# Kernel tuning notes

Measured on AMD Instinct MI355X. Metric: run time of the kernel, lower is better.

Reference implementation:

```python
import jax, jax.numpy as jnp
import numpy as np

N = 50000; E = 1600000; G = 512; HID = 128; H = 4; C = 32
NEG_SLOPE = 0.2


def _seg_softmax(scores, idx, n):
    # scores: [E, H], idx: [E] target nodes; softmax per target segment
    m = jax.ops.segment_max(scores, idx, num_segments=n)
    m = jnp.where(jnp.isfinite(m), m, 0.0)
    e = jnp.exp(scores - m[idx])
    s = jax.ops.segment_sum(e, idx, num_segments=n)
    return e / (s[idx] + 1e-16)


def setup_inputs() -> dict:
    key = jax.random.key(0)
    ks = jax.random.split(key, 32)
    nrm = lambda k, shape: jax.random.normal(k, shape, jnp.float32) * 0.05
    inp = {
        'x_nodes': jax.random.randint(ks[0], (N, 2), 0, 9, dtype=jnp.int32),
        'edge_index': jax.random.randint(ks[1], (2, E), 0, N, dtype=jnp.int32),
        'batch': jnp.sort(jax.random.randint(ks[2], (N,), 0, G, dtype=jnp.int32)),
        'num_graphs': G,
        'emb': nrm(ks[3], (9, 32)),
        'depth_emb': nrm(ks[4], (20, 32)),
        'proj_W': nrm(ks[5], (64, HID)),
        'proj_b': nrm(ks[6], (HID,)),
        'gat_W': nrm(ks[7], (3, HID, H * C)),
        'gat_att_src': nrm(ks[8], (3, H, C)),
        'gat_att_dst': nrm(ks[9], (3, H, C)),
        'gat_bias': nrm(ks[10], (3, HID)),
        'tr_Wq': nrm(ks[11], (HID, H * C)), 'tr_bq': nrm(ks[12], (H * C,)),
        'tr_Wk': nrm(ks[13], (HID, H * C)), 'tr_bk': nrm(ks[14], (H * C,)),
        'tr_Wv': nrm(ks[15], (HID, H * C)), 'tr_bv': nrm(ks[16], (H * C,)),
        'tr_Wskip': nrm(ks[17], (HID, HID)), 'tr_bskip': nrm(ks[18], (HID,)),
        'ln_g': jnp.ones((HID,), jnp.float32),
        'ln_b': jnp.zeros((HID,), jnp.float32),
    }
    return inp


def _forward(x_nodes, edge_index, batch, num_graphs, emb, depth_emb, proj_W, proj_b,
             gat_W, gat_att_src, gat_att_dst, gat_bias,
             tr_Wq, tr_bq, tr_Wk, tr_bk, tr_Wv, tr_bv, tr_Wskip, tr_bskip, ln_g, ln_b):
    n = x_nodes.shape[0]
    node_e = emb[x_nodes[:, 0]]                      # [N,32]
    depth_e = depth_emb[jnp.clip(x_nodes[:, 1], 0, 19)]  # [N,32]
    h = jnp.concatenate([node_e, depth_e], axis=1) @ proj_W + proj_b  # [N,128]

    # GATConv adds self-loops by default
    loops = jnp.arange(n, dtype=edge_index.dtype)
    src = jnp.concatenate([edge_index[0], loops])
    dst = jnp.concatenate([edge_index[1], loops])

    for l in range(3):
        hw = (h @ gat_W[l]).reshape(n, H, C)         # [N,H,C]
        a_src = (hw * gat_att_src[l]).sum(-1)        # [N,H]
        a_dst = (hw * gat_att_dst[l]).sum(-1)        # [N,H]
        scores = a_src[src] + a_dst[dst]             # [E+N,H]
        scores = jnp.where(scores >= 0, scores, NEG_SLOPE * scores)
        alpha = _seg_softmax(scores, dst, n)         # [E+N,H]
        msg = hw[src] * alpha[:, :, None]            # [E+N,H,C]
        out = jax.ops.segment_sum(msg, dst, num_segments=n).reshape(n, H * C)
        h = h + jax.nn.elu(out + gat_bias[l])

    # TransformerConv (no self-loops), root_weight=True
    tsrc, tdst = edge_index[0], edge_index[1]
    q = (h @ tr_Wq + tr_bq).reshape(n, H, C)
    k = (h @ tr_Wk + tr_bk).reshape(n, H, C)
    v = (h @ tr_Wv + tr_bv).reshape(n, H, C)
    scores = (q[tdst] * k[tsrc]).sum(-1) / jnp.sqrt(jnp.float32(C))  # [E,H]
    alpha = _seg_softmax(scores, tdst, n)
    agg = jax.ops.segment_sum(v[tsrc] * alpha[:, :, None], tdst, num_segments=n)
    h_trans = agg.reshape(n, H * C) + (h @ tr_Wskip + tr_bskip)
    h = h + jax.nn.elu(h_trans)

    # LayerNorm
    mu = h.mean(-1, keepdims=True)
    var = ((h - mu) ** 2).mean(-1, keepdims=True)
    h = (h - mu) * jax.lax.rsqrt(var + 1e-5) * ln_g + ln_b

    # global_mean_pool
    sums = jax.ops.segment_sum(h, batch, num_segments=num_graphs)
    cnt = jax.ops.segment_sum(jnp.ones((n,), h.dtype), batch, num_segments=num_graphs)
    return sums / jnp.maximum(cnt, 1.0)[:, None]


def reference(x_nodes, edge_index, batch, num_graphs, emb, depth_emb, proj_W, proj_b,
              gat_W, gat_att_src, gat_att_dst, gat_bias,
              tr_Wq, tr_bq, tr_Wk, tr_bk, tr_Wv, tr_bv, tr_Wskip, tr_bskip, ln_g, ln_b):
    return _forward(x_nodes, edge_index, batch, num_graphs, emb, depth_emb, proj_W, proj_b,
                    gat_W, gat_att_src, gat_att_dst, gat_bias,
                    tr_Wq, tr_bq, tr_Wk, tr_bk, tr_Wv, tr_bv, tr_Wskip, tr_bskip, ln_g, ln_b)
```

## Files before the change

kernel.cpp:

```cpp
#include <hip/hip_runtime.h>
#include <hip/hip_bf16.h>

typedef unsigned int uint;
typedef unsigned short ushort;
typedef __attribute__((ext_vector_type(8))) short bf16x8;
typedef __attribute__((ext_vector_type(4))) float f32x4;
typedef __attribute__((ext_vector_type(2))) float f32x2;

__device__ __forceinline__ float2 bf2_to_f2(uint u){
  union {unsigned int i; float f;} a,b;
  a.i = (u & 0xffffu) << 16;
  b.i = u & 0xffff0000u;
  return make_float2(a.f, b.f);
}
__device__ __forceinline__ float b2f(ushort u){
  union{uint i; float f;} x; x.i = (uint)u << 16; return x.f;
}
__device__ __forceinline__ ushort bf16bits(float f){
  union{ __hip_bfloat16 h; ushort u;} x; x.h = __float2bfloat16(f); return x.u;
}
__device__ __forceinline__ uint pack_bf2(float x, float y){
  return ((uint)bf16bits(y)<<16) | (uint)bf16bits(x);
}


__global__ void k_init_h(const int* __restrict__ xn, const float* __restrict__ table,
                         ushort* __restrict__ hb, int n){
  int gid = blockIdx.x*blockDim.x + threadIdx.x;
  if (gid >= n*64) return;
  int node = gid >> 6, lp = gid & 63;
  int x0 = xn[2*node];
  int x1 = xn[2*node+1]; x1 = x1<0?0:(x1>19?19:x1);
  const float* tr = table + (size_t)(x0*20+x1)*128 + lp*2;
  reinterpret_cast<uint*>(hb)[(size_t)node*64 + lp] = pack_bf2(tr[0], tr[1]);
}

__global__ void k_rank(const int* __restrict__ ei, int* __restrict__ cnt,
                       int* __restrict__ rank, int E){
  int e = blockIdx.x*blockDim.x + threadIdx.x;
  if (e >= E) return;
  rank[e] = atomicAdd(&cnt[ei[E+e]], 1);
}

__global__ __launch_bounds__(256) void k_scan_block(const int* __restrict__ deg, int* __restrict__ rowstart,
                                                    int* __restrict__ bsum, int n){
  int tid = threadIdx.x;
  int gid = blockIdx.x*256 + tid;
  int lane = tid & 63, wv = tid >> 6;
  int v = (gid < n) ? deg[gid] : 0;
  int x = v;
  #pragma unroll
  for (int off=1; off<64; off<<=1){
    int t = __shfl_up(x, off);
    if (lane >= off) x += t;
  }
  __shared__ int wsum[4], woff[4];
  if (lane==63) wsum[wv] = x;
  __syncthreads();
  if (tid==0){
    int r = 0;
    for (int i=0;i<4;++i){ woff[i]=r; r += wsum[i]; }
    bsum[blockIdx.x] = r;
  }
  __syncthreads();
  if (gid < n) rowstart[gid] = x + woff[wv] - v;
}

__global__ __launch_bounds__(256) void k_scan_sums(int* __restrict__ bsum, int nb){
  int tid = threadIdx.x;
  int lane = tid&63, wv = tid>>6;
  int v = (tid<nb)?bsum[tid]:0;
  int x = v;
  #pragma unroll
  for (int off=1;off<64;off<<=1){ int t=__shfl_up(x,off); if(lane>=off) x+=t; }
  __shared__ int wsum[4], woff[4];
  if (lane==63) wsum[wv]=x;
  __syncthreads();
  if (tid==0){ int r=0; for(int i=0;i<4;++i){woff[i]=r;r+=wsum[i];} }
  __syncthreads();
  if (tid<nb) bsum[tid] = x + woff[wv] - v;
}

__global__ void k_scan_add(int* __restrict__ rowstart, const int* __restrict__ bsum, int n, int total){
  int gid = blockIdx.x*256 + threadIdx.x;
  if (gid < n) rowstart[gid] += bsum[blockIdx.x];
  if (gid == 0) rowstart[n] = total;
}

__global__ void k_place(const int* __restrict__ ei, const int* __restrict__ rowstart,
                        const int* __restrict__ rank, ushort* __restrict__ csr16, int E){
  int e = blockIdx.x*blockDim.x + threadIdx.x;
  if (e >= E) return;
  csr16[rowstart[ei[E+e]] + rank[e]] = (ushort)ei[e];
}

__global__ __launch_bounds__(256) void k_prep_all(
    const float* __restrict__ gatW, const float* __restrict__ attS, const float* __restrict__ attD,
    const float* __restrict__ Wq, const float* __restrict__ Wk,
    const float* __restrict__ Wv, const float* __restrict__ Ws,
    const float* __restrict__ bq, const float* __restrict__ bk,
    const float* __restrict__ bv, const float* __restrict__ bs,
    const float* __restrict__ emb, const float* __restrict__ demb,
    const float* __restrict__ projW, const float* __restrict__ projB,
    ushort* __restrict__ wt_gat, ushort* __restrict__ wt_qkvs,
    float* __restrict__ bias512, float* __restrict__ table){
  int blk = blockIdx.x, t = threadIdx.x;
  if (blk < 192){
    int i = blk*256 + t;
    int l = i >> 14, rem = i & 16383, c = rem >> 7, k = rem & 127;
    wt_gat[(size_t)l*18432 + c*128 + k] = bf16bits(gatW[l*16384 + k*128 + c]);
  } else if (blk < 216){
    int idx = (blk-192)*256 + t;
    int l = idx >> 11, i16 = (idx >> 7) & 15, k = idx & 127;
    float acc = 0.f;
    if (i16 < 8){
      int sd = i16 >> 2, hh = i16 & 3;
      const float* att = (sd ? attD : attS) + l*128 + hh*32;
      #pragma unroll 8
      for (int c=0;c<32;++c) acc += gatW[l*16384 + k*128 + hh*32 + c] * att[c];
    }
    wt_gat[(size_t)l*18432 + (128+i16)*128 + k] = bf16bits(acc);
  } else if (blk < 472){
    int i = (blk-216)*256 + t;
    int c = i >> 7, k = i & 127;
    const float* W; const float* B; int sc; float scale = 1.f;
    if (c < 128){ W = Wq; B = bq; sc = c; scale = 0.011048543456039805f; }
    else if (c < 384){
      int ct = c >> 7, within = c & 127, cf = within >> 4, cl = within & 15;
      int m = cl + 16*((ct-1)*2 + (cf>>2));
      int wn = cf & 3;
      if (wn < 2){ W = Wk; B = bk; sc = 2*m + wn; }
      else       { W = Wv; B = bv; sc = 2*m + wn - 2; }
    } else { W = Ws; B = bs; sc = c - 384; }
    wt_qkvs[c*128 + k] = bf16bits(W[k*128 + sc] * scale);
    if (k == 0) bias512[c] = B[sc] * scale;
  } else {
    int idx = (blk-472)*256 + t;
    int combo = idx >> 7, d = idx & 127;
    int a = combo/20, b = combo - a*20;
    float acc = projB[d];
    #pragma unroll 8
    for (int i=0;i<32;++i) acc += emb[a*32+i]*projW[i*128+d];
    #pragma unroll 8
    for (int i=0;i<32;++i) acc += demb[b*32+i]*projW[(32+i)*128+d];
    table[combo*128+d] = acc;
  }
}

template<int CT, int MODE>
__global__ __launch_bounds__(256) void k_gemm_mfma(const ushort* __restrict__ X,
        const ushort* __restrict__ Wt, const float* __restrict__ bias,
        void* __restrict__ Yq, uint* __restrict__ Ykv, ushort* __restrict__ Ysk,
        float* __restrict__ Asd, int n){
  constexpr int COLS = (MODE==1) ? 144 : 128;
  constexpr int NCF  = COLS/16;
  __shared__ ushort wl[COLS*136];
  const int t = threadIdx.x;
  const int w = t >> 6, lane = t & 63;
  const int cl = lane & 15, khi = lane >> 4;
  const int rbase = blockIdx.x*64;

  int arow = rbase + w*16 + cl; if (arow >= n) arow = n-1;
  const bf16x8* Xr = reinterpret_cast<const bf16x8*>(X + (size_t)arow*128);
  bf16x8 a0 = Xr[0+khi], a1 = Xr[4+khi], a2 = Xr[8+khi], a3 = Xr[12+khi];

  for (int ct=0; ct<CT; ++ct){
    const ushort* wsrc = Wt + (size_t)ct*16384;
    __syncthreads();
    for (int idx = t; idx < COLS*2; idx += 256){
      int col = idx >> 1, k0 = (idx & 1)*64;
      const bf16x8* src = reinterpret_cast<const bf16x8*>(wsrc + (size_t)col*128 + k0);
      bf16x8* dst = reinterpret_cast<bf16x8*>(wl + col*136 + k0);
      #pragma unroll
      for (int i=0;i<8;++i) dst[i] = src[i];
    }
    __syncthreads();

    f32x4 acc[NCF];
    #pragma unroll
    for (int cf=0;cf<NCF;++cf) acc[cf] = f32x4{0.f,0.f,0.f,0.f};

    #pragma unroll
    for (int ks=0; ks<4; ++ks){
      bf16x8 av = (ks==0)?a0:(ks==1)?a1:(ks==2)?a2:a3;
      #pragma unroll
      for (int cf=0; cf<NCF; ++cf){
        bf16x8 bv = *reinterpret_cast<const bf16x8*>(wl + (cf*16+cl)*136 + ks*32 + khi*8);
        acc[cf] = __builtin_amdgcn_mfma_f32_16x16x32_bf16(av, bv, acc[cf], 0, 0, 0);
      }
    }

    #pragma unroll
    for (int j=0;j<4;++j){
      int node = rbase + w*16 + khi*4 + j;
      if (node < n){
        if (MODE==1){
          unsigned char* Y8 = (unsigned char*)Yq;
          float f0 = acc[0][j]*16.f, f1 = acc[1][j]*16.f, f2 = acc[2][j]*16.f, f3 = acc[3][j]*16.f;
          float f4 = acc[4][j]*16.f, f5 = acc[5][j]*16.f, f6 = acc[6][j]*16.f, f7 = acc[7][j]*16.f;
          int d0 = __builtin_amdgcn_cvt_pk_fp8_f32(f0, f1, 0, false);
          d0     = __builtin_amdgcn_cvt_pk_fp8_f32(f2, f3, d0, true);
          int d1 = __builtin_amdgcn_cvt_pk_fp8_f32(f4, f5, 0, false);
          d1     = __builtin_amdgcn_cvt_pk_fp8_f32(f6, f7, d1, true);
          *reinterpret_cast<uint2*>(Y8 + (size_t)node*128 + cl*8) = make_uint2((uint)d0, (uint)d1);
          if (cl < 8) Asd[(size_t)node*8 + cl] = acc[8][j];
        } else {
          if (ct == 0 || ct == 3){
            ushort* Y = (ct == 0) ? (ushort*)Yq : Ysk;
            ushort* yr = Y + (size_t)node*128 + cl;
            #pragma unroll
            for (int cf=0;cf<8;++cf)
              yr[cf*16] = bf16bits(acc[cf][j] + bias[ct*128 + cf*16 + cl]);
          } else {
            #pragma unroll
            for (int g=0; g<2; ++g){
              float f0 = (acc[g*4+0][j] + bias[ct*128 + (g*4+0)*16 + cl])*16.f;
              float f1 = (acc[g*4+1][j] + bias[ct*128 + (g*4+1)*16 + cl])*16.f;
              float f2 = (acc[g*4+2][j] + bias[ct*128 + (g*4+2)*16 + cl])*16.f;
              float f3 = (acc[g*4+3][j] + bias[ct*128 + (g*4+3)*16 + cl])*16.f;
              int d = __builtin_amdgcn_cvt_pk_fp8_f32(f0, f1, 0, false);
              d     = __builtin_amdgcn_cvt_pk_fp8_f32(f2, f3, d, true);
              int m = cl + 16*((ct-1)*2 + g);
              Ykv[(size_t)node*64 + m] = (uint)d;
            }
          }
        }
      }
    }
  }
}

__global__ __launch_bounds__(256) void k_gat_agg(const int* __restrict__ rowstart, const ushort* __restrict__ csr16,
              const unsigned char* __restrict__ hw8, const float* __restrict__ a_sd,
              const float* __restrict__ bias, ushort* __restrict__ hb, int n){
  __shared__ float4 lw[4][64];
  __shared__ ushort lsrc[4][64];
  int wv = threadIdx.x >> 6, l = threadIdx.x & 63;
  int node = blockIdx.x*4 + wv;
  if (node >= n) return;
  int b = l & 31, half = l >> 5;
  int h0 = (b & 1) * 2;
  int cl = b >> 1;
  int start = rowstart[node], end = rowstart[node+1];
  float4 ad4 = *reinterpret_cast<const float4*>(a_sd + (size_t)node*8 + 4);
  const uint* rows32 = reinterpret_cast<const uint*>(hw8);

  float a0=0.f,a1=0.f,a2=0.f,a3=0.f,sA=0.f,sB=0.f;
  if (half == 0){
    float adA = (h0==0) ? ad4.x : ad4.z;
    float adB = (h0==0) ? ad4.y : ad4.w;
    float scA = a_sd[(size_t)node*8 + h0]     + adA; scA = fmaxf(scA, 0.2f*scA);
    float scB = a_sd[(size_t)node*8 + h0 + 1] + adB; scB = fmaxf(scB, 0.2f*scB);
    float wA = __expf(fminf(scA,30.f));
    float wB = __expf(fminf(scB,30.f));
    uint u = rows32[(size_t)node*32 + b];
    f32x2 flo = __builtin_amdgcn_cvt_pk_f32_fp8((int)u, false);
    f32x2 fhi = __builtin_amdgcn_cvt_pk_f32_fp8((int)u, true);
    sA = wA; sB = wB;
    a0 = wA*flo.x; a1 = wA*flo.y; a2 = wB*fhi.x; a3 = wB*fhi.y;
  }

  const float* lwf = reinterpret_cast<const float*>(&lw[wv][0]);
  for (int base = start; base < end; base += 64){
    int len = end - base; if (len > 64) len = 64;
    if (l < len){
      int sv = csr16[base + l];
      lsrc[wv][l] = (ushort)sv;
      float4 a4 = *reinterpret_cast<const float4*>(a_sd + (size_t)sv*8);
      float s0 = a4.x + ad4.x; s0 = fmaxf(s0, 0.2f*s0);
      float s1 = a4.y + ad4.y; s1 = fmaxf(s1, 0.2f*s1);
      float s2 = a4.z + ad4.z; s2 = fmaxf(s2, 0.2f*s2);
      float s3 = a4.w + ad4.w; s3 = fmaxf(s3, 0.2f*s3);
      float4 w4;
      w4.x = __expf(fminf(s0,30.f));
      w4.y = __expf(fminf(s1,30.f));
      w4.z = __expf(fminf(s2,30.f));
      w4.w = __expf(fminf(s3,30.f));
      lw[wv][l] = w4;
    }
    int p = half;
    for (; p+6 < len; p += 8){
      int e0 = lsrc[wv][p], e1 = lsrc[wv][p+2], e2 = lsrc[wv][p+4], e3 = lsrc[wv][p+6];
      float2 w0 = *reinterpret_cast<const float2*>(lwf + p*4 + h0);
      float2 w1 = *reinterpret_cast<const float2*>(lwf + (p+2)*4 + h0);
      float2 w2 = *reinterpret_cast<const float2*>(lwf + (p+4)*4 + h0);
      float2 w3 = *reinterpret_cast<const float2*>(lwf + (p+6)*4 + h0);
      uint u0 = rows32[(size_t)e0*32 + b];
      uint u1 = rows32[(size_t)e1*32 + b];
      uint u2 = rows32[(size_t)e2*32 + b];
      uint u3 = rows32[(size_t)e3*32 + b];
      f32x2 f;
      f = __builtin_amdgcn_cvt_pk_f32_fp8((int)u0, false); a0 += w0.x*f.x; a1 += w0.x*f.y;
      f = __builtin_amdgcn_cvt_pk_f32_fp8((int)u0, true);  a2 += w0.y*f.x; a3 += w0.y*f.y;
      f = __builtin_amdgcn_cvt_pk_f32_fp8((int)u1, false); a0 += w1.x*f.x; a1 += w1.x*f.y;
      f = __builtin_amdgcn_cvt_pk_f32_fp8((int)u1, true);  a2 += w1.y*f.x; a3 += w1.y*f.y;
      f = __builtin_amdgcn_cvt_pk_f32_fp8((int)u2, false); a0 += w2.x*f.x; a1 += w2.x*f.y;
      f = __builtin_amdgcn_cvt_pk_f32_fp8((int)u2, true);  a2 += w2.y*f.x; a3 += w2.y*f.y;
      f = __builtin_amdgcn_cvt_pk_f32_fp8((int)u3, false); a0 += w3.x*f.x; a1 += w3.x*f.y;
      f = __builtin_amdgcn_cvt_pk_f32_fp8((int)u3, true);  a2 += w3.y*f.x; a3 += w3.y*f.y;
      sA += (w0.x+w1.x)+(w2.x+w3.x);
      sB += (w0.y+w1.y)+(w2.y+w3.y);
    }
    for (; p < len; p += 2){
      int e0 = lsrc[wv][p];
      float2 w0 = *reinterpret_cast<const float2*>(lwf + p*4 + h0);
      uint u0 = rows32[(size_t)e0*32 + b];
      f32x2 f;
      f = __builtin_amdgcn_cvt_pk_f32_fp8((int)u0, false); a0 += w0.x*f.x; a1 += w0.x*f.y;
      f = __builtin_amdgcn_cvt_pk_f32_fp8((int)u0, true);  a2 += w0.y*f.x; a3 += w0.y*f.y;
      sA += w0.x; sB += w0.y;
    }
  }
  a0 += __shfl_xor(a0,32); a1 += __shfl_xor(a1,32);
  a2 += __shfl_xor(a2,32); a3 += __shfl_xor(a3,32);
  sA += __shfl_xor(sA,32); sB += __shfl_xor(sB,32);
  float invA = (1.f/16.f)/(sA + 1e-16f);
  float invB = (1.f/16.f)/(sB + 1e-16f);
  float accx = half ? a2 : a0;
  float accy = half ? a3 : a1;
  float inv  = half ? invB : invA;
  int c0 = (h0*2 + half*2)*16 + cl;
  int c1 = c0 + 16;
  float o0 = accx*inv + bias[c0]; o0 = o0 > 0.f ? o0 : (__expf(o0)-1.f);
  float o1 = accy*inv + bias[c1]; o1 = o1 > 0.f ? o1 : (__expf(o1)-1.f);
  float hx = b2f(hb[(size_t)node*128 + c0]) + o0;
  float hy = b2f(hb[(size_t)node*128 + c1]) + o1;
  hb[(size_t)node*128 + c0] = bf16bits(hx);
  hb[(size_t)node*128 + c1] = bf16bits(hy);
}

__global__ __launch_bounds__(256) void k_trans_agg(const int* __restrict__ rowstart, const ushort* __restrict__ csr16,
              const ushort* __restrict__ yq, const uint* __restrict__ ykv,
              const ushort* __restrict__ ysk, const float* __restrict__ lng,
              const float* __restrict__ lnb, ushort* __restrict__ hb, int n){
  int wv = threadIdx.x>>6, lane = threadIdx.x&63;
  int node = blockIdx.x*4 + wv;
  if (node >= n) return;
  int li = lane & 15;
  bool odd1 = li & 1, odd2 = li & 2;
  int lbase = lane & 48;
  const uint* q32 = reinterpret_cast<const uint*>(yq);
  const uint* s32 = reinterpret_cast<const uint*>(ysk);
  uint* h32 = reinterpret_cast<uint*>(hb);
  float2 q2 = bf2_to_f2(q32[(size_t)node*64 + lane]);
  int start = rowstart[node], end = rowstart[node+1];
  float s = 0.f, s_tail = 0.f, ax = 0.f, ay = 0.f;
  int p = start;
  for (; p+7 < end; p += 8){
    int i0 = csr16[p],   i1 = csr16[p+1], i2 = csr16[p+2], i3 = csr16[p+3];
    int i4 = csr16[p+4], i5 = csr16[p+5], i6 = csr16[p+6], i7 = csr16[p+7];
    uint u0 = ykv[(size_t)i0*64 + lane];
    uint u1 = ykv[(size_t)i1*64 + lane];
    uint u2 = ykv[(size_t)i2*64 + lane];
    uint u3 = ykv[(size_t)i3*64 + lane];
    uint u4 = ykv[(size_t)i4*64 + lane];
    uint u5 = ykv[(size_t)i5*64 + lane];
    uint u6 = ykv[(size_t)i6*64 + lane];
    uint u7 = ykv[(size_t)i7*64 + lane];
    f32x2 k0 = __builtin_amdgcn_cvt_pk_f32_fp8((int)u0, false);
    f32x2 k1 = __builtin_amdgcn_cvt_pk_f32_fp8((int)u1, false);
    f32x2 k2 = __builtin_amdgcn_cvt_pk_f32_fp8((int)u2, false);
    f32x2 k3 = __builtin_amdgcn_cvt_pk_f32_fp8((int)u3, false);
    float p0 = q2.x*k0.x + q2.y*k0.y;
    float p1 = q2.x*k1.x + q2.y*k1.y;
    float p2 = q2.x*k2.x + q2.y*k2.y;
    float p3 = q2.x*k3.x + q2.y*k3.y;
    float aA = (odd1 ? p1 : p0) + __shfl_xor(odd1 ? p0 : p1, 1);
    float bA = (odd1 ? p3 : p2) + __shfl_xor(odd1 ? p2 : p3, 1);
    float cA = (odd2 ? bA : aA) + __shfl_xor(odd2 ? aA : bA, 2);
    cA += __shfl_xor(cA, 4);
    cA += __shfl_xor(cA, 8);
    float wA = __expf(fminf(cA, 30.f));
    f32x2 k4 = __builtin_amdgcn_cvt_pk_f32_fp8((int)u4, false);
    f32x2 k5 = __builtin_amdgcn_cvt_pk_f32_fp8((int)u5, false);
    f32x2 k6 = __builtin_amdgcn_cvt_pk_f32_fp8((int)u6, false);
    f32x2 k7 = __builtin_amdgcn_cvt_pk_f32_fp8((int)u7, false);
    float p4 = q2.x*k4.x + q2.y*k4.y;
    float p5 = q2.x*k5.x + q2.y*k5.y;
    float p6 = q2.x*k6.x + q2.y*k6.y;
    float p7 = q2.x*k7.x + q2.y*k7.y;
    float aB = (odd1 ? p5 : p4) + __shfl_xor(odd1 ? p4 : p5, 1);
    float bB = (odd1 ? p7 : p6) + __shfl_xor(odd1 ? p6 : p7, 1);
    float cB = (odd2 ? bB : aB) + __shfl_xor(odd2 ? aB : bB, 2);
    cB += __shfl_xor(cB, 4);
    cB += __shfl_xor(cB, 8);
    float wB = __expf(fminf(cB, 30.f));
    s += wA + wB;
    float w0 = __shfl(wA, lbase);
    float w1 = __shfl(wA, lbase|1);
    float w2 = __shfl(wA, lbase|2);
    float w3 = __shfl(wA, lbase|3);
    float w4 = __shfl(wB, lbase);
    float w5 = __shfl(wB, lbase|1);
    float w6 = __shfl(wB, lbase|2);
    float w7 = __shfl(wB, lbase|3);
    f32x2 v0 = __builtin_amdgcn_cvt_pk_f32_fp8((int)u0, true);
    f32x2 v1 = __builtin_amdgcn_cvt_pk_f32_fp8((int)u1, true);
    f32x2 v2 = __builtin_amdgcn_cvt_pk_f32_fp8((int)u2, true);
    f32x2 v3 = __builtin_amdgcn_cvt_pk_f32_fp8((int)u3, true);
    f32x2 v4 = __builtin_amdgcn_cvt_pk_f32_fp8((int)u4, true);
    f32x2 v5 = __builtin_amdgcn_cvt_pk_f32_fp8((int)u5, true);
    f32x2 v6 = __builtin_amdgcn_cvt_pk_f32_fp8((int)u6, true);
    f32x2 v7 = __builtin_amdgcn_cvt_pk_f32_fp8((int)u7, true);
    ax += w0*v0.x + w1*v1.x + w2*v2.x + w3*v3.x
        + w4*v4.x + w5*v5.x + w6*v6.x + w7*v7.x;
    ay += w0*v0.y + w1*v1.y + w2*v2.y + w3*v3.y
        + w4*v4.y + w5*v5.y + w6*v6.y + w7*v7.y;
  }
  for (; p+3 < end; p += 4){
    int i0 = csr16[p], i1 = csr16[p+1], i2 = csr16[p+2], i3 = csr16[p+3];
    uint u0 = ykv[(size_t)i0*64 + lane];
    uint u1 = ykv[(size_t)i1*64 + lane];
    uint u2 = ykv[(size_t)i2*64 + lane];
    uint u3 = ykv[(size_t)i3*64 + lane];
    f32x2 k0 = __builtin_amdgcn_cvt_pk_f32_fp8((int)u0, false);
    f32x2 k1 = __builtin_amdgcn_cvt_pk_f32_fp8((int)u1, false);
    f32x2 k2 = __builtin_amdgcn_cvt_pk_f32_fp8((int)u2, false);
    f32x2 k3 = __builtin_amdgcn_cvt_pk_f32_fp8((int)u3, false);
    float p0 = q2.x*k0.x + q2.y*k0.y;
    float p1 = q2.x*k1.x + q2.y*k1.y;
    float p2 = q2.x*k2.x + q2.y*k2.y;
    float p3 = q2.x*k3.x + q2.y*k3.y;
    float aA = (odd1 ? p1 : p0) + __shfl_xor(odd1 ? p0 : p1, 1);
    float bA = (odd1 ? p3 : p2) + __shfl_xor(odd1 ? p2 : p3, 1);
    float cA = (odd2 ? bA : aA) + __shfl_xor(odd2 ? aA : bA, 2);
    cA += __shfl_xor(cA, 4);
    cA += __shfl_xor(cA, 8);
    float w = __expf(fminf(cA, 30.f));
    s += w;
    float w0 = __shfl(w, lbase);
    float w1 = __shfl(w, lbase|1);
    float w2 = __shfl(w, lbase|2);
    float w3 = __shfl(w, lbase|3);
    f32x2 v0 = __builtin_amdgcn_cvt_pk_f32_fp8((int)u0, true);
    f32x2 v1 = __builtin_amdgcn_cvt_pk_f32_fp8((int)u1, true);
    f32x2 v2 = __builtin_amdgcn_cvt_pk_f32_fp8((int)u2, true);
    f32x2 v3 = __builtin_amdgcn_cvt_pk_f32_fp8((int)u3, true);
    ax += w0*v0.x + w1*v1.x + w2*v2.x + w3*v3.x;
    ay += w0*v0.y + w1*v1.y + w2*v2.y + w3*v3.y;
  }
  for (; p < end; ++p){
    int idx = csr16[p];
    uint u = ykv[(size_t)idx*64 + lane];
    f32x2 k2 = __builtin_amdgcn_cvt_pk_f32_fp8((int)u, false);
    float pr = q2.x*k2.x + q2.y*k2.y;
    pr += __shfl_xor(pr,1); pr += __shfl_xor(pr,2);
    pr += __shfl_xor(pr,4); pr += __shfl_xor(pr,8);
    float wt = __expf(fminf(pr, 30.f));
    f32x2 v2 = __builtin_amdgcn_cvt_pk_f32_fp8((int)u, true);
    s_tail += wt; ax += wt*v2.x; ay += wt*v2.y;
  }
  s += __shfl_xor(s, 1);
  s += __shfl_xor(s, 2);
  s += s_tail;
  float inv = (1.f/16.f)/(s + 1e-16f);
  int d = lane*2;
  float2 sk = bf2_to_f2(s32[(size_t)node*64 + lane]);
  float tx = ax*inv + sk.x;
  float ty = ay*inv + sk.y;
  tx = tx>0.f?tx:(__expf(tx)-1.f);
  ty = ty>0.f?ty:(__expf(ty)-1.f);
  float2 hp = bf2_to_f2(h32[(size_t)node*64 + lane]);
  hp.x += tx; hp.y += ty;
  float sm = hp.x + hp.y;
  #pragma unroll
  for (int m=1;m<64;m<<=1) sm += __shfl_xor(sm,m);
  float mu = sm * (1.f/128.f);
  float dx = hp.x-mu, dy = hp.y-mu;
  float vs = dx*dx + dy*dy;
  #pragma unroll
  for (int m=1;m<64;m<<=1) vs += __shfl_xor(vs,m);
  float r = rsqrtf(vs*(1.f/128.f) + 1e-5f);
  float2 gg = *reinterpret_cast<const float2*>(lng+d);
  float2 bb = *reinterpret_cast<const float2*>(lnb+d);
  h32[(size_t)node*64 + lane] = pack_bf2(dx*r*gg.x + bb.x, dy*r*gg.y + bb.y);
}

__global__ void k_pool(const ushort* __restrict__ hb, const int* __restrict__ batch,
                       float* __restrict__ out, int n, int G){
  int g = blockIdx.x, t = threadIdx.x;
  int lo=0, hi=n;
  while (lo<hi){ int m=(lo+hi)>>1; if (batch[m] < g) lo=m+1; else hi=m; }
  int s = lo;
  lo=s; hi=n;
  while (lo<hi){ int m=(lo+hi)>>1; if (batch[m] < g+1) lo=m+1; else hi=m; }
  int e = lo;
  const uint* rows = reinterpret_cast<const uint*>(hb);
  float ax=0.f, ay=0.f;
  for (int i=s;i<e;++i){
    float2 f = bf2_to_f2(rows[(size_t)i*64 + t]);
    ax += f.x; ay += f.y;
  }
  float invc = 1.f / fmaxf((float)(e-s), 1.f);
  out[(size_t)g*128 + 2*t]   = ax*invc;
  out[(size_t)g*128 + 2*t+1] = ay*invc;
}

extern "C" void kernel_launch(void* const* d_in, const int* in_sizes, int n_in,
                              void* d_out, int out_size, void* d_ws, size_t ws_size,
                              hipStream_t stream){
  const int* xn    = (const int*)d_in[0];
  const int* ei    = (const int*)d_in[1];
  const int* batch = (const int*)d_in[2];
  const float* emb  = (const float*)d_in[4];
  const float* demb = (const float*)d_in[5];
  const float* projW= (const float*)d_in[6];
  const float* projB= (const float*)d_in[7];
  const float* gatW = (const float*)d_in[8];
  const float* attS = (const float*)d_in[9];
  const float* attD = (const float*)d_in[10];
  const float* gatB = (const float*)d_in[11];
  const float* Wq = (const float*)d_in[12];
  const float* bq = (const float*)d_in[13];
  const float* Wk = (const float*)d_in[14];
  const float* bk = (const float*)d_in[15];
  const float* Wv = (const float*)d_in[16];
  const float* bv = (const float*)d_in[17];
  const float* Wsk= (const float*)d_in[18];
  const float* bsk= (const float*)d_in[19];
  const float* lng= (const float*)d_in[20];
  const float* lnb= (const float*)d_in[21];
  float* out = (float*)d_out;

  int N = in_sizes[0]/2;
  int E = in_sizes[1]/2;
  int G = out_size/128;

  char* w = (char*)d_ws;
  size_t off = 0;
  auto alloc = [&](size_t bytes)->char*{ char* p = w+off; off += (bytes + 255) & ~(size_t)255; return p; };
  ushort* hb   = (ushort*)alloc((size_t)N*128*2);
  ushort* yq   = (ushort*)alloc((size_t)N*128*2);
  uint*   ykv  = (uint*)  alloc((size_t)N*64*4);
  ushort* ysk  = (ushort*)alloc((size_t)N*128*2);
  unsigned char* hw8 = (unsigned char*)yq;
  float* a_sd = (float*)alloc((size_t)N*8*4);
  int* cnt    = (int*)alloc((size_t)N*4);
  int* rowstart=(int*)alloc((size_t)(N+1)*4);
  int* rank   = (int*)alloc((size_t)E*4);
  ushort* csr16 = (ushort*)alloc((size_t)E*2);
  int* bsum   = (int*)alloc(4096);
  float* table= (float*)alloc(180*128*4);
  ushort* wt_gat  = (ushort*)alloc((size_t)3*144*128*2);
  ushort* wt_qkvs = (ushort*)alloc((size_t)512*128*2);
  float* bias512  = (float*)alloc(512*4);
  (void)ws_size; (void)n_in;

  int nb = (N+255)/256;

  hipMemsetAsync(cnt, 0, (size_t)N*4, stream);
  k_prep_all<<<562,256,0,stream>>>(gatW, attS, attD, Wq, Wk, Wv, Wsk,
                                   bq, bk, bv, bsk, emb, demb, projW, projB,
                                   wt_gat, wt_qkvs, bias512, table);
  k_init_h<<<(N*64+255)/256,256,0,stream>>>(xn, table, hb, N);
  k_rank<<<(E+255)/256,256,0,stream>>>(ei, cnt, rank, E);
  k_scan_block<<<nb,256,0,stream>>>(cnt, rowstart, bsum, N);
  k_scan_sums<<<1,256,0,stream>>>(bsum, nb);
  k_scan_add<<<nb,256,0,stream>>>(rowstart, bsum, N, E);
  k_place<<<(E+255)/256,256,0,stream>>>(ei, rowstart, rank, csr16, E);

  int gemm_grid = (N+63)/64;
  for (int l=0;l<3;++l){
    k_gemm_mfma<1,1><<<gemm_grid,256,0,stream>>>(hb, wt_gat + (size_t)l*18432, nullptr,
                                                 hw8, nullptr, nullptr, a_sd, N);
    k_gat_agg<<<(N+3)/4,256,0,stream>>>(rowstart, csr16, hw8, a_sd, gatB + l*128, hb, N);
  }

  k_gemm_mfma<4,2><<<gemm_grid,256,0,stream>>>(hb, wt_qkvs, bias512, yq, ykv, ysk, nullptr, N);
  k_trans_agg<<<(N+3)/4,256,0,stream>>>(rowstart, csr16, yq, ykv, ysk, lng, lnb, hb, N);

  k_pool<<<G,64,0,stream>>>(hb, batch, out, N, G);
}
```

Measured before the change: 408.0 us.

## Build CSR via two-pass bucketed radix sort with shared-memory atomics

Replaces the global-atomic rank plus scatter CSR construction with a two-level bucket sort. Edges are first histogrammed by the high byte of dst in shared memory and scattered into coarse buckets, then each bucket is locally counted, scanned and placed using shared-memory atomics. This removes the N-sized global atomic counters and the random global scatter, at the cost of an extra edge buffer pass. It assumes node ids fit within 256 buckets of 256 (N ≤ 65536).

```diff
diff --git a/kernel.cpp b/kernel.cpp
--- a/kernel.cpp
+++ b/kernel.cpp
@@ -35,11 +35,17 @@
   reinterpret_cast<uint*>(hb)[(size_t)node*64 + lp] = pack_bf2(tr[0], tr[1]);
 }
 
-__global__ void k_rank(const int* __restrict__ ei, int* __restrict__ cnt,
-                       int* __restrict__ rank, int E){
-  int e = blockIdx.x*blockDim.x + threadIdx.x;
-  if (e >= E) return;
-  rank[e] = atomicAdd(&cnt[ei[E+e]], 1);
+__global__ __launch_bounds__(256) void k_bhist(const int* __restrict__ ei, int* __restrict__ scanarr, int E){
+  __shared__ int h[256];
+  h[threadIdx.x] = 0;
+  __syncthreads();
+  int chunk = (E + 255) >> 8;
+  int s = blockIdx.x*chunk;
+  int e = s + chunk; if (e > E) e = E;
+  for (int i = s + threadIdx.x; i < e; i += 256)
+    atomicAdd(&h[ei[E+i] >> 8], 1);
+  __syncthreads();
+  scanarr[threadIdx.x*256 + blockIdx.x] = h[threadIdx.x];
 }
 
 __global__ __launch_bounds__(256) void k_scan_block(const int* __restrict__ deg, int* __restrict__ rowstart,
@@ -87,11 +93,58 @@
   if (gid == 0) rowstart[n] = total;
 }
 
-__global__ void k_place(const int* __restrict__ ei, const int* __restrict__ rowstart,
-                        const int* __restrict__ rank, ushort* __restrict__ csr16, int E){
-  int e = blockIdx.x*blockDim.x + threadIdx.x;
-  if (e >= E) return;
-  csr16[rowstart[ei[E+e]] + rank[e]] = (ushort)ei[e];
+__global__ __launch_bounds__(256) void k_bscatter(const int* __restrict__ ei, const int* __restrict__ scanarr,
+                                                  uint* __restrict__ ebuf, int E){
+  __shared__ int cur[256];
+  cur[threadIdx.x] = scanarr[threadIdx.x*256 + blockIdx.x];
+  __syncthreads();
+  int chunk = (E + 255) >> 8;
+  int s = blockIdx.x*chunk;
+  int e = s + chunk; if (e > E) e = E;
+  for (int i = s + threadIdx.x; i < e; i += 256){
+    int dst = ei[E+i], src = ei[i];
+    int pos = atomicAdd(&cur[dst >> 8], 1);
+    ebuf[pos] = ((uint)dst << 16) | (uint)src;
+  }
+}
+
+__global__ __launch_bounds__(256) void k_bbuild(const uint* __restrict__ ebuf, const int* __restrict__ scanarr,
+                                                int* __restrict__ rowstart, ushort* __restrict__ csr16,
+                                                int E, int N){
+  __shared__ int cnt[256];
+  __shared__ int cur[256];
+  __shared__ int wsum[4], woff[4];
+  int t = threadIdx.x, b = blockIdx.x;
+  int s = scanarr[b*256];
+  int e = scanarr[(b+1)*256];
+  cnt[t] = 0;
+  __syncthreads();
+  for (int i = s + t; i < e; i += 256)
+    atomicAdd(&cnt[(ebuf[i] >> 16) & 255], 1);
+  __syncthreads();
+  int lane = t & 63, wv = t >> 6;
+  int v = cnt[t];
+  int x = v;
+  #pragma unroll
+  for (int off=1; off<64; off<<=1){
+    int tt = __shfl_up(x, off);
+    if (lane >= off) x += tt;
+  }
+  if (lane==63) wsum[wv] = x;
+  __syncthreads();
+  if (t==0){ int r=0; for (int i=0;i<4;++i){ woff[i]=r; r+=wsum[i]; } }
+  __syncthreads();
+  int pref = x + woff[wv] - v;
+  int d = b*256 + t;
+  if (d < N) rowstart[d] = s + pref;
+  if (b==0 && t==0) rowstart[N] = E;
+  cur[t] = s + pref;
+  __syncthreads();
+  for (int i = s + t; i < e; i += 256){
+    uint ev = ebuf[i];
+    int pos = atomicAdd(&cur[(ev >> 16) & 255], 1);
+    csr16[pos] = (ushort)(ev & 0xffffu);
+  }
 }
 
 __global__ __launch_bounds__(256) void k_prep_all(
@@ -535,9 +588,9 @@
   ushort* ysk  = (ushort*)alloc((size_t)N*128*2);
   unsigned char* hw8 = (unsigned char*)yq;
   float* a_sd = (float*)alloc((size_t)N*8*4);
-  int* cnt    = (int*)alloc((size_t)N*4);
   int* rowstart=(int*)alloc((size_t)(N+1)*4);
-  int* rank   = (int*)alloc((size_t)E*4);
+  uint* ebuf  = (uint*)alloc((size_t)E*4);
+  int* scanarr= (int*)alloc((size_t)(256*256+1)*4);
   ushort* csr16 = (ushort*)alloc((size_t)E*2);
   int* bsum   = (int*)alloc(4096);
   float* table= (float*)alloc(180*128*4);
@@ -546,18 +599,16 @@
   float* bias512  = (float*)alloc(512*4);
   (void)ws_size; (void)n_in;
 
-  int nb = (N+255)/256;
-
-  hipMemsetAsync(cnt, 0, (size_t)N*4, stream);
+  k_bhist<<<256,256,0,stream>>>(ei, scanarr, E);
   k_prep_all<<<562,256,0,stream>>>(gatW, attS, attD, Wq, Wk, Wv, Wsk,
                                    bq, bk, bv, bsk, emb, demb, projW, projB,
                                    wt_gat, wt_qkvs, bias512, table);
   k_init_h<<<(N*64+255)/256,256,0,stream>>>(xn, table, hb, N);
-  k_rank<<<(E+255)/256,256,0,stream>>>(ei, cnt, rank, E);
-  k_scan_block<<<nb,256,0,stream>>>(cnt, rowstart, bsum, N);
-  k_scan_sums<<<1,256,0,stream>>>(bsum, nb);
-  k_scan_add<<<nb,256,0,stream>>>(rowstart, bsum, N, E);
-  k_place<<<(E+255)/256,256,0,stream>>>(ei, rowstart, rank, csr16, E);
+  k_scan_block<<<256,256,0,stream>>>(scanarr, scanarr, bsum, 256*256);
+  k_scan_sums<<<1,256,0,stream>>>(bsum, 256);
+  k_scan_add<<<256,256,0,stream>>>(scanarr, bsum, 256*256, E);
+  k_bscatter<<<256,256,0,stream>>>(ei, scanarr, ebuf, E);
+  k_bbuild<<<256,256,0,stream>>>(ebuf, scanarr, rowstart, csr16, E, N);
 
   int gemm_grid = (N+63)/64;
   for (int l=0;l<3;++l){
```

Result: faster. 352.1 us (median of 2 runs) (-13.7%).
